# Performance work log

Measured on AMD Instinct MI355X. Metric: run time of the kernel, lower is better.

Reference implementation:

```python
import jax, jax.numpy as jnp
import numpy as np

N_HEAD, D_MODEL, D_HEAD, D_INNER = 16, 1024, 64, 4096
QLEN, BSZ = 2048, 2
LN_EPS = 1e-5
NEG_MIN = np.float32(np.finfo(np.float32).min)


def layer_norm(x, g, b, eps=LN_EPS):
    mu = jnp.mean(x, axis=-1, keepdims=True)
    var = jnp.var(x, axis=-1, keepdims=True)
    return (x - mu) * jax.lax.rsqrt(var + eps) * g + b


def rel_shift_uni(x):
    # x: [q, k, b, n] -> Transformer-XL relative shift
    q, k, b, n = x.shape
    zero_pad = jnp.zeros((q, 1, b, n), dtype=x.dtype)
    x_padded = jnp.concatenate([zero_pad, x], axis=1)        # [q, k+1, b, n]
    x_padded = x_padded.reshape(k + 1, q, b, n)
    return x_padded[1:].reshape(q, k, b, n)


def setup_inputs() -> dict:
    key = jax.random.key(0)
    ks = jax.random.split(key, 16)
    s = 0.02
    inp = {
        "dec_inp": jax.random.normal(ks[0], (QLEN, BSZ, D_MODEL), jnp.float32),
        "r": jax.random.normal(ks[1], (QLEN, D_MODEL), jnp.float32),
        "r_w_bias": jax.random.normal(ks[2], (N_HEAD, D_HEAD), jnp.float32) * s,
        "r_r_bias": jax.random.normal(ks[3], (N_HEAD, D_HEAD), jnp.float32) * s,
        "qkv_w": jax.random.normal(ks[4], (3 * N_HEAD * D_HEAD, D_MODEL), jnp.float32) * s,
        "r_net_w": jax.random.normal(ks[5], (N_HEAD * D_HEAD, D_MODEL), jnp.float32) * s,
        "o_w": jax.random.normal(ks[6], (D_MODEL, N_HEAD * D_HEAD), jnp.float32) * s,
        "ln_attn_g": jnp.ones((D_MODEL,), jnp.float32),
        "ln_attn_b": jnp.zeros((D_MODEL,), jnp.float32),
        "w1": jax.random.normal(ks[7], (D_INNER, D_MODEL), jnp.float32) * s,
        "b1": jnp.zeros((D_INNER,), jnp.float32),
        "w2": jax.random.normal(ks[8], (D_MODEL, D_INNER), jnp.float32) * s,
        "b2": jnp.zeros((D_MODEL,), jnp.float32),
        "ln_ff_g": jnp.ones((D_MODEL,), jnp.float32),
        "ln_ff_b": jnp.zeros((D_MODEL,), jnp.float32),
        # causal mask: mask position j > i; shape [q, k, 1]
        "attn_mask": jnp.triu(jnp.ones((QLEN, QLEN), bool), k=1)[:, :, None],
    }
    return inp


def reference(dec_inp, r, r_w_bias, r_r_bias, qkv_w, r_net_w, o_w,
              ln_attn_g, ln_attn_b, w1, b1, w2, b2, ln_ff_g, ln_ff_b,
              attn_mask):
    qlen, bsz = dec_inp.shape[0], dec_inp.shape[1]
    scale = 1.0 / (D_HEAD ** 0.5)

    # QKV projection (post-LN: no pre-norm)
    w_heads = jnp.einsum('ibm,hm->ibh', dec_inp, qkv_w)  # [q, b, 3*n*d]
    w_head_q, w_head_k, w_head_v = jnp.split(w_heads, 3, axis=-1)
    w_head_q = w_head_q.reshape(qlen, bsz, N_HEAD, D_HEAD)
    w_head_k = w_head_k.reshape(qlen, bsz, N_HEAD, D_HEAD)
    w_head_v = w_head_v.reshape(qlen, bsz, N_HEAD, D_HEAD)

    # content attention score (AC)
    rw_head_q = w_head_q + r_w_bias                      # [q, b, n, d]
    attn_score = jnp.einsum('ibnd,jbnd->ijbn', rw_head_q, w_head_k)

    # position attention score (BD) with relative shift
    rr_head_q = w_head_q + r_r_bias
    r_head_k = jnp.einsum('jm,hm->jh', r, r_net_w).reshape(qlen, N_HEAD, D_HEAD)
    BD = jnp.einsum('ibnd,jnd->ijbn', rr_head_q, r_head_k)
    BD = rel_shift_uni(BD)

    attn_score = (attn_score + BD) * scale
    attn_score = jnp.where(attn_mask[:, :, :, None], NEG_MIN, attn_score)

    attn_prob = jax.nn.softmax(attn_score, axis=1)       # softmax over key dim
    attn_vec = jnp.einsum('ijbn,jbnd->ibnd', attn_prob, w_head_v)
    attn_vec = attn_vec.reshape(qlen, bsz, N_HEAD * D_HEAD)
    attn_out = jnp.einsum('ibh,mh->ibm', attn_vec, o_w)

    # post-LN residual
    output = layer_norm(dec_inp + attn_out, ln_attn_g, ln_attn_b)

    # Positionwise FFN (post-LN)
    hidden = jax.nn.relu(jnp.einsum('ibm,fm->ibf', output, w1) + b1)
    core_out = jnp.einsum('ibf,mf->ibm', hidden, w2) + b2
    output = layer_norm(output + core_out, ln_ff_g, ln_ff_b)
    return output
```

## Files before the change

kernel.cpp:

```cpp
#include <hip/hip_runtime.h>
#include <stdint.h>

#define QL 2048
#define NHEAD 16
#define DHEAD 64
#define DMODEL 1024
#define DINNER 4096

typedef __attribute__((ext_vector_type(8))) short bf16x8;
typedef __attribute__((ext_vector_type(4))) float f32x4;

__device__ __forceinline__ ushort f2bf(float f) {
  uint32_t u = __float_as_uint(f);
  u = (u + 0x7fffu + ((u >> 16) & 1u)) >> 16;
  return (ushort)u;
}
__device__ __forceinline__ float bf2f(ushort u) {
  return __uint_as_float(((uint32_t)u) << 16);
}

__device__ __forceinline__ void gload_lds16(const void* g, void* l) {
  auto gp = reinterpret_cast<const uint32_t __attribute__((address_space(1)))*>(
      reinterpret_cast<uintptr_t>(g));
  auto lp = reinterpret_cast<uint32_t __attribute__((address_space(3)))*>(
      (uint32_t)reinterpret_cast<uintptr_t>(l));
  __builtin_amdgcn_global_load_lds(gp, lp, 16, 0, 0);
}

__global__ __launch_bounds__(256) void cvt_bf16_k(const float* __restrict__ in,
                                                  ushort* __restrict__ out, int n4) {
  int i = blockIdx.x * 256 + threadIdx.x;
  if (i < n4) {
    float4 v = ((const float4*)in)[i];
    ushort4 u;
    u.x = f2bf(v.x); u.y = f2bf(v.y); u.z = f2bf(v.z); u.w = f2bf(v.w);
    ((ushort4*)out)[i] = u;
  }
}

#define EPI_QKV 0
#define EPI_RK 1
#define EPI_F32 2
#define EPI_RELU_BF16 3
#define EPI_BIAS_F32 4

template <int EPI>
__global__ __launch_bounds__(256) void gemm_nt(
    const ushort* __restrict__ A, const ushort* __restrict__ B, int M, int N, int K,
    float* __restrict__ Cf, ushort* __restrict__ Cb, const float* __restrict__ bias,
    ushort* __restrict__ qw, ushort* __restrict__ qr, ushort* __restrict__ kbuf,
    ushort* __restrict__ vt, const float* __restrict__ rwb, const float* __restrict__ rrb) {
  __shared__ ushort As[128 * 32];
  __shared__ ushort Bs[128 * 32];
  const int t = threadIdx.x;
  const int lane = t & 63, wv = t >> 6;
  const int wr = wv >> 1, wc = wv & 1;
  const int m0 = blockIdx.y * 128, n0 = blockIdx.x * 128;
  const int rif = lane & 15;
  const int kb = (lane >> 4) * 16;

  f32x4 acc[4][4] = {};
  const char* Ab = (const char*)A;
  const char* Bb = (const char*)B;
  const int arow = t >> 2;
  const int acol = (t & 3) * 16;

  for (int k0 = 0; k0 < K; k0 += 32) {
    __syncthreads();
    {
      size_t abase = ((size_t)(m0 + arow) * K + k0) * 2 + acol;
      gload_lds16(Ab + abase, (char*)As + t * 16);
      gload_lds16(Ab + abase + (size_t)64 * K * 2, (char*)As + t * 16 + 4096);
      size_t bbase = ((size_t)(n0 + arow) * K + k0) * 2 + acol;
      gload_lds16(Bb + bbase, (char*)Bs + t * 16);
      gload_lds16(Bb + bbase + (size_t)64 * K * 2, (char*)Bs + t * 16 + 4096);
    }
    __syncthreads();
    bf16x8 af[4], bfr[4];
#pragma unroll
    for (int m = 0; m < 4; m++)
      af[m] = *(const bf16x8*)((const char*)As + (wr * 64 + m * 16 + rif) * 64 + kb);
#pragma unroll
    for (int n = 0; n < 4; n++)
      bfr[n] = *(const bf16x8*)((const char*)Bs + (wc * 64 + n * 16 + rif) * 64 + kb);
#pragma unroll
    for (int m = 0; m < 4; m++)
#pragma unroll
      for (int n = 0; n < 4; n++)
        acc[m][n] = __builtin_amdgcn_mfma_f32_16x16x32_bf16(af[m], bfr[n], acc[m][n], 0, 0, 0);
  }

  const int rbase = (lane >> 4) * 4;
#pragma unroll
  for (int m = 0; m < 4; m++) {
#pragma unroll
    for (int n = 0; n < 4; n++) {
#pragma unroll
      for (int reg = 0; reg < 4; reg++) {
        int gr = m0 + wr * 64 + m * 16 + rbase + reg;
        int gc = n0 + wc * 64 + n * 16 + (lane & 15);
        float v = acc[m][n][reg];
        if (EPI == EPI_F32) {
          Cf[(size_t)gr * N + gc] = v;
        } else if (EPI == EPI_BIAS_F32) {
          Cf[(size_t)gr * N + gc] = v + bias[gc];
        } else if (EPI == EPI_RELU_BF16) {
          Cb[(size_t)gr * N + gc] = f2bf(fmaxf(v + bias[gc], 0.f));
        } else if (EPI == EPI_RK) {
          int hn = gc >> 6, hd = gc & 63;
          Cb[((size_t)hn * QL + gr) * 64 + hd] = f2bf(v);
        } else {
          int which = gc >> 10, hh = gc & 1023;
          int hn = hh >> 6, hd = hh & 63;
          int qi = gr >> 1, qb = gr & 1;
          size_t off = ((size_t)(qb * NHEAD + hn) * QL + qi) * 64 + hd;
          if (which == 0) {
            qw[off] = f2bf(v + rwb[hh]);
            qr[off] = f2bf(v + rrb[hh]);
          } else if (which == 1) {
            kbuf[off] = f2bf(v);
          } else {
            vt[((size_t)(qb * NHEAD + hn) * 64 + hd) * QL + qi] = f2bf(v);
          }
        }
      }
    }
  }
}

template <int EPI>
__global__ __launch_bounds__(256) void gemm_nt64(
    const ushort* __restrict__ A, const ushort* __restrict__ B, int M, int N, int K,
    float* __restrict__ Cf, ushort* __restrict__ Cb, const float* __restrict__ bias) {
  __shared__ ushort As[128 * 32];
  __shared__ ushort Bs[64 * 32];
  const int t = threadIdx.x;
  const int lane = t & 63, wv = t >> 6;
  const int wr = wv >> 1, wc = wv & 1;
  const int m0 = blockIdx.y * 128, n0 = blockIdx.x * 64;
  const int rif = lane & 15;
  const int kb = (lane >> 4) * 16;

  f32x4 acc[4][2] = {};
  const char* Ab = (const char*)A;
  const char* Bb = (const char*)B;
  const int arow = t >> 2;
  const int acol = (t & 3) * 16;

  for (int k0 = 0; k0 < K; k0 += 32) {
    __syncthreads();
    {
      size_t abase = ((size_t)(m0 + arow) * K + k0) * 2 + acol;
      gload_lds16(Ab + abase, (char*)As + t * 16);
      gload_lds16(Ab + abase + (size_t)64 * K * 2, (char*)As + t * 16 + 4096);
      size_t bbase = ((size_t)(n0 + arow) * K + k0) * 2 + acol;
      gload_lds16(Bb + bbase, (char*)Bs + t * 16);
    }
    __syncthreads();
    bf16x8 af[4], bfr[2];
#pragma unroll
    for (int m = 0; m < 4; m++)
      af[m] = *(const bf16x8*)((const char*)As + (wr * 64 + m * 16 + rif) * 64 + kb);
#pragma unroll
    for (int n = 0; n < 2; n++)
      bfr[n] = *(const bf16x8*)((const char*)Bs + (wc * 32 + n * 16 + rif) * 64 + kb);
#pragma unroll
    for (int m = 0; m < 4; m++)
#pragma unroll
      for (int n = 0; n < 2; n++)
        acc[m][n] = __builtin_amdgcn_mfma_f32_16x16x32_bf16(af[m], bfr[n], acc[m][n], 0, 0, 0);
  }

  const int rbase = (lane >> 4) * 4;
#pragma unroll
  for (int m = 0; m < 4; m++) {
#pragma unroll
    for (int n = 0; n < 2; n++) {
#pragma unroll
      for (int reg = 0; reg < 4; reg++) {
        int gr = m0 + wr * 64 + m * 16 + rbase + reg;
        int gc = n0 + wc * 32 + n * 16 + (lane & 15);
        float v = acc[m][n][reg];
        if (EPI == EPI_F32) {
          Cf[(size_t)gr * N + gc] = v;
        } else if (EPI == EPI_BIAS_F32) {
          Cf[(size_t)gr * N + gc] = v + bias[gc];
        } else {
          int hn = gc >> 6, hd = gc & 63;
          Cb[((size_t)hn * QL + gr) * 64 + hd] = f2bf(v);
        }
      }
    }
  }
}

__global__ __launch_bounds__(256) void flash_attn(
    const ushort* __restrict__ Qw, const ushort* __restrict__ Qr,
    const ushort* __restrict__ Kb, const ushort* __restrict__ Vt,
    const ushort* __restrict__ Rk, ushort* __restrict__ out) {
  __shared__ ushort K_lds[2][64 * 64];
  __shared__ ushort V_lds[2][64 * 64];
  __shared__ ushort R_lds[2][128 * 64];
  __shared__ ushort P_lds[4][16 * 64];

  const int t = threadIdx.x;
  const int lane = t & 63, wv = t >> 6;
  const int bn = blockIdx.y;
  const int qb = bn >> 4, hn = bn & 15;
  const int c4 = lane & 15, g4 = lane >> 4;

  const char* Qwb = (const char*)(Qw + (size_t)bn * QL * 64);
  const char* Qrb = (const char*)(Qr + (size_t)bn * QL * 64);
  const char* Kbb = (const char*)(Kb + (size_t)bn * QL * 64);
  const char* Vtb = (const char*)(Vt + (size_t)bn * 64 * QL);
  const char* Rkb = (const char*)(Rk + (size_t)hn * QL * 64);

  int addrs[4];
#pragma unroll
  for (int reg = 0; reg < 4; reg++) {
    int rr = g4 * 4 + reg;
    addrs[reg] = ((lane & 48) | ((c4 + 15 - rr) & 15)) << 2;
  }

  const float SCALE2 = 0.125f * 1.44269504088896340736f;

#pragma unroll 1
  for (int ph = 0; ph < 2; ph++) {
    const int itile = (ph == 0) ? (31 - (int)blockIdx.x) : (int)blockIdx.x;
    const int i0 = itile * 64;
    const int iw = i0 + wv * 16;
    const int niter = itile + 1;

    bf16x8 qwf[2], qrf[2];
#pragma unroll
    for (int kk = 0; kk < 2; kk++) {
      qwf[kk] = *(const bf16x8*)(Qwb + (size_t)(iw + c4) * 128 + kk * 64 + g4 * 16);
      qrf[kk] = *(const bf16x8*)(Qrb + (size_t)(iw + c4) * 128 + kk * 64 + g4 * 16);
    }

    f32x4 o_acc[4] = {};
    float m_run[4], l_run[4];
#pragma unroll
    for (int r = 0; r < 4; r++) { m_run[r] = -3.0e38f; l_run[r] = 0.f; }

    auto stage = [&](int b, int j0) {
      const int T0 = j0 - i0 + (QL - 64);
#pragma unroll
      for (int p = 0; p < 2; p++) {
        int o = t * 16 + p * 4096;
        int row = o >> 7, ch16 = ((((o & 127) >> 4) ^ (row & 7)) << 4);
        gload_lds16(Kbb + (size_t)(j0 + row) * 128 + ch16, (char*)K_lds[b] + o);
        gload_lds16(Vtb + (size_t)row * (QL * 2) + (size_t)j0 * 2 + ch16, (char*)V_lds[b] + o);
      }
#pragma unroll
      for (int p = 0; p < 4; p++) {
        int o = t * 16 + p * 4096;
        int r = o >> 7;
        int srow = T0 + r; srow = srow > QL - 1 ? QL - 1 : srow;
        int ch16 = ((((o & 127) >> 4) ^ (r & 7)) << 4);
        gload_lds16(Rkb + (size_t)srow * 128 + ch16, (char*)R_lds[b] + o);
      }
    };

    stage(0, 0);
    asm volatile("s_waitcnt vmcnt(0)" ::: "memory");
    __builtin_amdgcn_s_barrier();
    __builtin_amdgcn_sched_barrier(0);

    int cur = 0;
#pragma unroll 1
    for (int it = 0; it < niter; ++it) {
      const int j0 = it * 64;
      if (it + 1 < niter) stage(cur ^ 1, j0 + 64);

      f32x4 acc_s[4] = {};
      f32x4 acc_bd[5] = {};
      const int baseloc = 48 - wv * 16;
      __builtin_amdgcn_s_setprio(1);
#pragma unroll
      for (int kk = 0; kk < 2; kk++) {
        const int sw = (((kk * 4 + g4) ^ (c4 & 7)) << 4);
#pragma unroll
        for (int nf = 0; nf < 4; nf++) {
          bf16x8 bk = *(const bf16x8*)((const char*)K_lds[cur] + (nf * 16 + c4) * 128 + sw);
          acc_s[nf] = __builtin_amdgcn_mfma_f32_16x16x32_bf16(qwf[kk], bk, acc_s[nf], 0, 0, 0);
        }
#pragma unroll
        for (int tf = 0; tf < 5; tf++) {
          int oo = baseloc + tf * 16 + c4;
          bf16x8 br = *(const bf16x8*)((const char*)R_lds[cur] + oo * 128 + sw);
          acc_bd[tf] = __builtin_amdgcn_mfma_f32_16x16x32_bf16(qrf[kk], br, acc_bd[tf], 0, 0, 0);
        }
      }
      __builtin_amdgcn_s_setprio(0);

      uint32_t pk[4][4];
#pragma unroll
      for (int nf = 0; nf < 4; nf++)
#pragma unroll
        for (int reg = 0; reg < 4; reg++)
          asm("v_cvt_pk_bf16_f32 %0, %1, %2"
              : "=v"(pk[nf][reg])
              : "v"(acc_bd[nf][reg]), "v"(acc_bd[nf + 1][reg]));

      float sv[4][4];
      float rowmax[4] = {-3.0e38f, -3.0e38f, -3.0e38f, -3.0e38f};
#pragma unroll
      for (int nf = 0; nf < 4; nf++) {
#pragma unroll
        for (int reg = 0; reg < 4; reg++) {
          int rr = g4 * 4 + reg;
          int jg = j0 + nf * 16 + c4;
          int ig = iw + rr;
          uint32_t pulled = (uint32_t)__builtin_amdgcn_ds_bpermute(addrs[reg], (int)pk[nf][reg]);
          uint32_t bits = (c4 > rr) ? (pulled & 0xffff0000u) : (pulled << 16);
          float v = (acc_s[nf][reg] + __uint_as_float(bits)) * SCALE2;
          v = (jg <= ig) ? v : -3.0e38f;
          sv[nf][reg] = v;
          rowmax[reg] = fmaxf(rowmax[reg], v);
        }
      }
#pragma unroll
      for (int reg = 0; reg < 4; reg++) {
        float rm = rowmax[reg];
        rm = fmaxf(rm, __shfl_xor(rm, 1));
        rm = fmaxf(rm, __shfl_xor(rm, 2));
        rm = fmaxf(rm, __shfl_xor(rm, 4));
        rm = fmaxf(rm, __shfl_xor(rm, 8));
        float mnew = fmaxf(m_run[reg], rm);
        float alpha = __builtin_amdgcn_exp2f(m_run[reg] - mnew);
        float rsum = 0.f;
#pragma unroll
        for (int nf = 0; nf < 4; nf++) {
          float p = __builtin_amdgcn_exp2f(sv[nf][reg] - mnew);
          sv[nf][reg] = p;
          rsum += p;
        }
        rsum += __shfl_xor(rsum, 1);
        rsum += __shfl_xor(rsum, 2);
        rsum += __shfl_xor(rsum, 4);
        rsum += __shfl_xor(rsum, 8);
        l_run[reg] = l_run[reg] * alpha + rsum;
        m_run[reg] = mnew;
#pragma unroll
        for (int df = 0; df < 4; df++) o_acc[df][reg] *= alpha;
      }

      {
        char* pb = (char*)P_lds[wv];
#pragma unroll
        for (int nf = 0; nf < 4; nf++)
#pragma unroll
          for (int reg = 0; reg < 4; reg++) {
            int row = g4 * 4 + reg, col = nf * 16 + c4;
            int byt = row * 128 + ((((col >> 3) ^ (row & 7))) << 4) + (col & 7) * 2;
            *(ushort*)(pb + byt) = f2bf(sv[nf][reg]);
          }
      }
      __builtin_amdgcn_s_setprio(1);
#pragma unroll
      for (int kk = 0; kk < 2; kk++) {
        const char* pb = (const char*)P_lds[wv];
        bf16x8 pa = *(const bf16x8*)(pb + c4 * 128 + (((kk * 4 + g4) ^ (c4 & 7)) << 4));
        const int sw = (((kk * 4 + g4) ^ (c4 & 7)) << 4);
#pragma unroll
        for (int df = 0; df < 4; df++) {
          bf16x8 bv = *(const bf16x8*)((const char*)V_lds[cur] + (df * 16 + c4) * 128 + sw);
          o_acc[df] = __builtin_amdgcn_mfma_f32_16x16x32_bf16(pa, bv, o_acc[df], 0, 0, 0);
        }
      }
      __builtin_amdgcn_s_setprio(0);

      asm volatile("s_waitcnt vmcnt(0)" ::: "memory");
      __builtin_amdgcn_s_barrier();
      __builtin_amdgcn_sched_barrier(0);
      cur ^= 1;
    }

#pragma unroll
    for (int reg = 0; reg < 4; reg++) {
      float inv = 1.0f / l_run[reg];
      int ig = iw + g4 * 4 + reg;
      size_t grow = (size_t)(ig * 2 + qb) * 1024 + hn * 64;
#pragma unroll
      for (int df = 0; df < 4; df++)
        out[grow + df * 16 + c4] = f2bf(o_acc[df][reg] * inv);
    }
  }
}

template <bool WB>
__global__ __launch_bounds__(256) void ln_res(
    const float* __restrict__ xa, const float* __restrict__ xb,
    const float* __restrict__ g, const float* __restrict__ bt,
    float* __restrict__ of, ushort* __restrict__ ob) {
  __shared__ float red[8];
  const int row = blockIdx.x;
  const int t = threadIdx.x;
  const int lane = t & 63, wv = t >> 6;
  const float4 a = *(const float4*)(xa + (size_t)row * 1024 + t * 4);
  const float4 c = *(const float4*)(xb + (size_t)row * 1024 + t * 4);
  float x[4] = {a.x + c.x, a.y + c.y, a.z + c.z, a.w + c.w};
  float s = x[0] + x[1] + x[2] + x[3];
  for (int m = 1; m < 64; m <<= 1) s += __shfl_xor(s, m);
  if (lane == 0) red[wv] = s;
  __syncthreads();
  float mu = (red[0] + red[1] + red[2] + red[3]) * (1.f / 1024.f);
  float d[4];
  float ss = 0.f;
#pragma unroll
  for (int i = 0; i < 4; i++) { d[i] = x[i] - mu; ss += d[i] * d[i]; }
  for (int m = 1; m < 64; m <<= 1) ss += __shfl_xor(ss, m);
  if (lane == 0) red[4 + wv] = ss;
  __syncthreads();
  float var = (red[4] + red[5] + red[6] + red[7]) * (1.f / 1024.f);
  float rs = rsqrtf(var + 1e-5f);
  float4 gv = *(const float4*)(g + t * 4);
  float4 bv = *(const float4*)(bt + t * 4);
  float y[4] = {d[0] * rs * gv.x + bv.x, d[1] * rs * gv.y + bv.y,
                d[2] * rs * gv.z + bv.z, d[3] * rs * gv.w + bv.w};
  float4 yo = make_float4(y[0], y[1], y[2], y[3]);
  *(float4*)(of + (size_t)row * 1024 + t * 4) = yo;
  if (WB) {
    ushort4 u;
    u.x = f2bf(y[0]); u.y = f2bf(y[1]); u.z = f2bf(y[2]); u.w = f2bf(y[3]);
    *(ushort4*)(ob + (size_t)row * 1024 + t * 4) = u;
  }
}

extern "C" void kernel_launch(void* const* d_in, const int* in_sizes, int n_in,
                              void* d_out, int out_size, void* d_ws, size_t ws_size,
                              hipStream_t stream) {
  const float* dec_inp = (const float*)d_in[0];
  const float* r_in = (const float*)d_in[1];
  const float* rwb = (const float*)d_in[2];
  const float* rrb = (const float*)d_in[3];
  const float* qkv_w = (const float*)d_in[4];
  const float* rnet_w = (const float*)d_in[5];
  const float* o_w = (const float*)d_in[6];
  const float* ln_attn_g = (const float*)d_in[7];
  const float* ln_attn_b = (const float*)d_in[8];
  const float* w1 = (const float*)d_in[9];
  const float* b1 = (const float*)d_in[10];
  const float* w2 = (const float*)d_in[11];
  const float* b2 = (const float*)d_in[12];
  const float* ln_ff_g = (const float*)d_in[13];
  const float* ln_ff_b = (const float*)d_in[14];
  float* out = (float*)d_out;

  char* ws = (char*)d_ws;
  size_t off = 0;
  auto alloc = [&](size_t bytes) {
    char* p = ws + off;
    off += (bytes + 255) & ~(size_t)255;
    return p;
  };
  const int ROWS = QL * 2;
  ushort* qkvw_b = (ushort*)alloc((size_t)3072 * 1024 * 2);
  ushort* rnetw_b = (ushort*)alloc((size_t)1024 * 1024 * 2);
  ushort* ow_b = (ushort*)alloc((size_t)1024 * 1024 * 2);
  ushort* w1_b = (ushort*)alloc((size_t)4096 * 1024 * 2);
  ushort* w2_b = (ushort*)alloc((size_t)1024 * 4096 * 2);
  ushort* x_b = (ushort*)alloc((size_t)ROWS * 1024 * 2);
  ushort* r_b = (ushort*)alloc((size_t)QL * 1024 * 2);
  ushort* Qw = (ushort*)alloc((size_t)32 * QL * 64 * 2);
  ushort* Qr = (ushort*)alloc((size_t)32 * QL * 64 * 2);
  ushort* Kb = (ushort*)alloc((size_t)32 * QL * 64 * 2);
  ushort* Vt = (ushort*)alloc((size_t)32 * 64 * QL * 2);
  ushort* rk = (ushort*)alloc((size_t)16 * QL * 64 * 2);
  ushort* avec = (ushort*)alloc((size_t)ROWS * 1024 * 2);
  float* attn_out = (float*)alloc((size_t)ROWS * 1024 * 4);
  float* x1f = (float*)alloc((size_t)ROWS * 1024 * 4);
  ushort* x1b = (ushort*)alloc((size_t)ROWS * 1024 * 2);
  ushort* hidden = (ushort*)alloc((size_t)ROWS * 4096 * 2);
  float* core = (float*)alloc((size_t)ROWS * 1024 * 4);

  auto cvt = [&](const float* src, ushort* dst, int n) {
    int n4 = n / 4;
    cvt_bf16_k<<<n4 / 256, 256, 0, stream>>>(src, dst, n4);
  };
  cvt(qkv_w, qkvw_b, 3072 * 1024);
  cvt(rnet_w, rnetw_b, 1024 * 1024);
  cvt(o_w, ow_b, 1024 * 1024);
  cvt(w1, w1_b, 4096 * 1024);
  cvt(w2, w2_b, 1024 * 4096);
  cvt(dec_inp, x_b, ROWS * 1024);
  cvt(r_in, r_b, QL * 1024);

  gemm_nt<EPI_QKV><<<dim3(3072 / 128, ROWS / 128), 256, 0, stream>>>(
      x_b, qkvw_b, ROWS, 3072, 1024, nullptr, nullptr, nullptr, Qw, Qr, Kb, Vt, rwb, rrb);
  gemm_nt64<EPI_RK><<<dim3(1024 / 64, QL / 128), 256, 0, stream>>>(
      r_b, rnetw_b, QL, 1024, 1024, nullptr, rk, nullptr);
  flash_attn<<<dim3(16, 32), 256, 0, stream>>>(Qw, Qr, Kb, Vt, rk, avec);
  gemm_nt64<EPI_F32><<<dim3(1024 / 64, ROWS / 128), 256, 0, stream>>>(
      avec, ow_b, ROWS, 1024, 1024, attn_out, nullptr, nullptr);
  ln_res<true><<<ROWS, 256, 0, stream>>>(dec_inp, attn_out, ln_attn_g, ln_attn_b, x1f, x1b);
  gemm_nt<EPI_RELU_BF16><<<dim3(4096 / 128, ROWS / 128), 256, 0, stream>>>(
      x1b, w1_b, ROWS, 4096, 1024, nullptr, hidden, b1, nullptr, nullptr, nullptr, nullptr,
      nullptr, nullptr);
  gemm_nt64<EPI_BIAS_F32><<<dim3(1024 / 64, ROWS / 128), 256, 0, stream>>>(
      hidden, w2_b, ROWS, 1024, 4096, core, nullptr, b2);
  ln_res<false><<<ROWS, 256, 0, stream>>>(x1f, core, ln_ff_g, ln_ff_b, out, nullptr);
}
```

Baseline: 377.9 us.

## Double-buffer LDS tiles in GEMM kernels to overlap global loads with MFMA

Both GEMM kernels now use two LDS buffers per operand and prefetch the next K-slice with direct global-to-LDS loads while MFMAs consume the current one. The two __syncthreads per iteration become one explicit vmcnt wait plus barrier, and s_setprio raises wave priority around the MFMA block. The aim is to hide global load latency behind compute. In exchange LDS use per block doubles, which can lower occupancy, and the full vmcnt(0) wait each iteration still limits how far loads can run ahead.

```diff
diff --git a/kernel.cpp b/kernel.cpp
--- a/kernel.cpp
+++ b/kernel.cpp
@@ -50,8 +50,8 @@
     float* __restrict__ Cf, ushort* __restrict__ Cb, const float* __restrict__ bias,
     ushort* __restrict__ qw, ushort* __restrict__ qr, ushort* __restrict__ kbuf,
     ushort* __restrict__ vt, const float* __restrict__ rwb, const float* __restrict__ rrb) {
-  __shared__ ushort As[128 * 32];
-  __shared__ ushort Bs[128 * 32];
+  __shared__ ushort As[2][128 * 32];
+  __shared__ ushort Bs[2][128 * 32];
   const int t = threadIdx.x;
   const int lane = t & 63, wv = t >> 6;
   const int wr = wv >> 1, wc = wv & 1;
@@ -65,29 +65,42 @@
   const int arow = t >> 2;
   const int acol = (t & 3) * 16;
 
+  auto stage = [&](int b, int k0) {
+    size_t abase = ((size_t)(m0 + arow) * K + k0) * 2 + acol;
+    gload_lds16(Ab + abase, (char*)As[b] + t * 16);
+    gload_lds16(Ab + abase + (size_t)64 * K * 2, (char*)As[b] + t * 16 + 4096);
+    size_t bbase = ((size_t)(n0 + arow) * K + k0) * 2 + acol;
+    gload_lds16(Bb + bbase, (char*)Bs[b] + t * 16);
+    gload_lds16(Bb + bbase + (size_t)64 * K * 2, (char*)Bs[b] + t * 16 + 4096);
+  };
+
+  stage(0, 0);
+  asm volatile("s_waitcnt vmcnt(0)" ::: "memory");
+  __builtin_amdgcn_s_barrier();
+  __builtin_amdgcn_sched_barrier(0);
+
+  int cur = 0;
+#pragma unroll 1
   for (int k0 = 0; k0 < K; k0 += 32) {
-    __syncthreads();
-    {
-      size_t abase = ((size_t)(m0 + arow) * K + k0) * 2 + acol;
-      gload_lds16(Ab + abase, (char*)As + t * 16);
-      gload_lds16(Ab + abase + (size_t)64 * K * 2, (char*)As + t * 16 + 4096);
-      size_t bbase = ((size_t)(n0 + arow) * K + k0) * 2 + acol;
-      gload_lds16(Bb + bbase, (char*)Bs + t * 16);
-      gload_lds16(Bb + bbase + (size_t)64 * K * 2, (char*)Bs + t * 16 + 4096);
-    }
-    __syncthreads();
+    if (k0 + 32 < K) stage(cur ^ 1, k0 + 32);
     bf16x8 af[4], bfr[4];
 #pragma unroll
     for (int m = 0; m < 4; m++)
-      af[m] = *(const bf16x8*)((const char*)As + (wr * 64 + m * 16 + rif) * 64 + kb);
+      af[m] = *(const bf16x8*)((const char*)As[cur] + (wr * 64 + m * 16 + rif) * 64 + kb);
 #pragma unroll
     for (int n = 0; n < 4; n++)
-      bfr[n] = *(const bf16x8*)((const char*)Bs + (wc * 64 + n * 16 + rif) * 64 + kb);
+      bfr[n] = *(const bf16x8*)((const char*)Bs[cur] + (wc * 64 + n * 16 + rif) * 64 + kb);
+    __builtin_amdgcn_s_setprio(1);
 #pragma unroll
     for (int m = 0; m < 4; m++)
 #pragma unroll
       for (int n = 0; n < 4; n++)
         acc[m][n] = __builtin_amdgcn_mfma_f32_16x16x32_bf16(af[m], bfr[n], acc[m][n], 0, 0, 0);
+    __builtin_amdgcn_s_setprio(0);
+    asm volatile("s_waitcnt vmcnt(0)" ::: "memory");
+    __builtin_amdgcn_s_barrier();
+    __builtin_amdgcn_sched_barrier(0);
+    cur ^= 1;
   }
 
   const int rbase = (lane >> 4) * 4;
@@ -132,8 +145,8 @@
 __global__ __launch_bounds__(256) void gemm_nt64(
     const ushort* __restrict__ A, const ushort* __restrict__ B, int M, int N, int K,
     float* __restrict__ Cf, ushort* __restrict__ Cb, const float* __restrict__ bias) {
-  __shared__ ushort As[128 * 32];
-  __shared__ ushort Bs[64 * 32];
+  __shared__ ushort As[2][128 * 32];
+  __shared__ ushort Bs[2][64 * 32];
   const int t = threadIdx.x;
   const int lane = t & 63, wv = t >> 6;
   const int wr = wv >> 1, wc = wv & 1;
@@ -147,28 +160,41 @@
   const int arow = t >> 2;
   const int acol = (t & 3) * 16;
 
+  auto stage = [&](int b, int k0) {
+    size_t abase = ((size_t)(m0 + arow) * K + k0) * 2 + acol;
+    gload_lds16(Ab + abase, (char*)As[b] + t * 16);
+    gload_lds16(Ab + abase + (size_t)64 * K * 2, (char*)As[b] + t * 16 + 4096);
+    size_t bbase = ((size_t)(n0 + arow) * K + k0) * 2 + acol;
+    gload_lds16(Bb + bbase, (char*)Bs[b] + t * 16);
+  };
+
+  stage(0, 0);
+  asm volatile("s_waitcnt vmcnt(0)" ::: "memory");
+  __builtin_amdgcn_s_barrier();
+  __builtin_amdgcn_sched_barrier(0);
+
+  int cur = 0;
+#pragma unroll 1
   for (int k0 = 0; k0 < K; k0 += 32) {
-    __syncthreads();
-    {
-      size_t abase = ((size_t)(m0 + arow) * K + k0) * 2 + acol;
-      gload_lds16(Ab + abase, (char*)As + t * 16);
-      gload_lds16(Ab + abase + (size_t)64 * K * 2, (char*)As + t * 16 + 4096);
-      size_t bbase = ((size_t)(n0 + arow) * K + k0) * 2 + acol;
-      gload_lds16(Bb + bbase, (char*)Bs + t * 16);
-    }
-    __syncthreads();
+    if (k0 + 32 < K) stage(cur ^ 1, k0 + 32);
     bf16x8 af[4], bfr[2];
 #pragma unroll
     for (int m = 0; m < 4; m++)
-      af[m] = *(const bf16x8*)((const char*)As + (wr * 64 + m * 16 + rif) * 64 + kb);
+      af[m] = *(const bf16x8*)((const char*)As[cur] + (wr * 64 + m * 16 + rif) * 64 + kb);
 #pragma unroll
     for (int n = 0; n < 2; n++)
-      bfr[n] = *(const bf16x8*)((const char*)Bs + (wc * 32 + n * 16 + rif) * 64 + kb);
+      bfr[n] = *(const bf16x8*)((const char*)Bs[cur] + (wc * 32 + n * 16 + rif) * 64 + kb);
+    __builtin_amdgcn_s_setprio(1);
 #pragma unroll
     for (int m = 0; m < 4; m++)
 #pragma unroll
       for (int n = 0; n < 2; n++)
         acc[m][n] = __builtin_amdgcn_mfma_f32_16x16x32_bf16(af[m], bfr[n], acc[m][n], 0, 0, 0);
+    __builtin_amdgcn_s_setprio(0);
+    asm volatile("s_waitcnt vmcnt(0)" ::: "memory");
+    __builtin_amdgcn_s_barrier();
+    __builtin_amdgcn_sched_barrier(0);
+    cur ^= 1;
   }
 
   const int rbase = (lane >> 4) * 4;
```

Result: faster. 358.4 us (-5.2%).
